# Kernel tuning notes

Hardware: AMD Instinct MI355X
Metric: run time of the kernel (lower is better)

Reference implementation:

```python
import jax, jax.numpy as jnp
import numpy as np

C_NUM, D_NUM = 64, 128
N_NODES = C_NUM * D_NUM + C_NUM + D_NUM  # 8384
HEADS, OUT = 4, 256


def gat_conv(h, src, dst, W, al, ar, b):
    """DGL-style GATConv (eval mode, attn_drop off). h:[N,F], W:[F,H*O], al/ar:[H,O], b:[H*O]."""
    N = h.shape[0]
    H, O = al.shape
    feat = (h @ W).reshape(N, H, O)
    el = jnp.sum(feat * al, axis=-1)                      # [N,H]
    er = jnp.sum(feat * ar, axis=-1)
    e = jax.nn.leaky_relu(el[src] + er[dst], 0.2)         # [E,H]
    m = jax.ops.segment_max(e, dst, num_segments=N)
    m = jnp.where(jnp.isfinite(m), m, 0.0)
    p = jnp.exp(e - m[dst])
    s = jax.ops.segment_sum(p, dst, num_segments=N)
    a = p / jnp.maximum(s[dst], 1e-9)                     # edge softmax per dst, per head
    out = jax.ops.segment_sum(a[:, :, None] * feat[src], dst, num_segments=N)  # [N,H,O]
    return out + b.reshape(1, H, O)


def cagat_layer(edges, dfeat, cvec, gw, al, ar, gb,
                wq_w, wq_b, wk_w, wk_b, wv_w, wv_b, ip_w, ip_b, op_w, op_b):
    ch = cvec.shape[1]
    pad = jnp.repeat(cvec, D_NUM, axis=0)                       # [c*d, ch]
    pad3 = jnp.broadcast_to(cvec.mean(axis=0), (D_NUM, ch))      # [d, ch]
    cfin = jnp.concatenate([pad, cvec, pad3], axis=0)            # [N, ch]
    inf = jnp.concatenate([dfeat, cfin], axis=1)                 # [N, F+ch]
    # 4 relation-specific GATConvs, stacked (HeteroGraphConv aggregate='stack')
    rst = jnp.stack([gat_conv(inf, edges[t, 0], edges[t, 1], gw[t], al[t], ar[t], gb[t])
                     for t in range(4)], axis=1)                 # [N,4,H,O]
    N = inf.shape[0]
    rst = rst.reshape(N, 4 * HEADS, OUT)
    E = OUT
    Q = (cfin @ wq_w + wq_b)[:, None, :]                         # [N,1,E]
    K = rst @ wk_w + wk_b                                        # [N,16,E]
    V = rst @ wv_w + wv_b
    # nn.MultiheadAttention(E, 1): in-proj then single-head SDPA then out-proj
    q = Q @ ip_w[:E].T + ip_b[:E]
    k = K @ ip_w[E:2 * E].T + ip_b[E:2 * E]
    v = V @ ip_w[2 * E:].T + ip_b[2 * E:]
    att = jax.nn.softmax(jnp.einsum('nqe,nke->nqk', q, k) / jnp.sqrt(jnp.float32(E)), axis=-1)
    o = jnp.einsum('nqk,nke->nqe', att, v) @ op_w.T + op_b
    return o.reshape(N, E)


def setup_inputs() -> dict:
    key = jax.random.key(0)
    ks = iter(jax.random.split(key, 64))
    rn = lambda shape: jax.random.normal(next(ks), shape, jnp.float32) * 0.05
    inp = {}
    inp['x'] = rn((D_NUM, 256))
    inp['cf'] = rn((C_NUM, 512))
    inp['cf_net_w'] = rn((512, 128)); inp['cf_net_b'] = rn((128,))
    inp['ht_w'] = rn((512, 256)); inp['ht_b'] = rn((256,))
    for l in ('1', '2'):
        inp['gw' + l] = rn((4, 384, HEADS * OUT))
        inp['al' + l] = rn((4, HEADS, OUT))
        inp['ar' + l] = rn((4, HEADS, OUT))
        inp['gb' + l] = rn((4, HEADS * OUT))
        inp['wq' + l + '_w'] = rn((128, 256)); inp['wq' + l + '_b'] = rn((256,))
        inp['wk' + l + '_w'] = rn((256, 256)); inp['wk' + l + '_b'] = rn((256,))
        inp['wv' + l + '_w'] = rn((256, 256)); inp['wv' + l + '_b'] = rn((256,))
        inp['ip' + l + '_w'] = rn((768, 256)); inp['ip' + l + '_b'] = rn((768,))
        inp['op' + l + '_w'] = rn((256, 256)); inp['op' + l + '_b'] = rn((256,))
    inp['edges'] = jax.random.randint(next(ks), (4, 2, 50000), 0, N_NODES, dtype=jnp.int32)
    return inp


def reference(x, cf, cf_net_w, cf_net_b, ht_w, ht_b,
              gw1, al1, ar1, gb1, wq1_w, wq1_b, wk1_w, wk1_b, wv1_w, wv1_b, ip1_w, ip1_b, op1_w, op1_b,
              gw2, al2, ar2, gb2, wq2_w, wq2_b, wk2_w, wk2_b, wv2_w, wv2_b, ip2_w, ip2_b, op2_w, op2_b,
              edges):
    cf_vec = cf @ cf_net_w + cf_net_b                           # [c, cell_hidden]
    d_pad = jnp.tile(x, (C_NUM, 1))                             # [c*d, in]
    d_uc = cf @ ht_w + ht_b                                     # [c, in]
    d_feat = jnp.concatenate([d_pad, d_uc, x], axis=0)          # [N, in]
    h = cagat_layer(edges, d_feat, cf_vec, gw1, al1, ar1, gb1,
                    wq1_w, wq1_b, wk1_w, wk1_b, wv1_w, wv1_b, ip1_w, ip1_b, op1_w, op1_b)
    h = cagat_layer(edges, h, cf_vec, gw2, al2, ar2, gb2,
                    wq2_w, wq2_b, wk2_w, wk2_b, wv2_w, wv2_b, ip2_w, ip2_b, op2_w, op2_b)
    return h
```

## Files before the change

### kernel.cpp

```cpp
#include <hip/hip_runtime.h>
#include <hip/hip_bf16.h>

typedef __hip_bfloat16 bf16;
typedef __attribute__((ext_vector_type(8))) short short8;
typedef __attribute__((ext_vector_type(4))) short short4v;
typedef __attribute__((ext_vector_type(4))) float f32x4;

#define KN 8384
#define KNPAD 8448
#define KE 50000
#define NBIG 4480

__device__ __forceinline__ float toF(float v){ return v; }
__device__ __forceinline__ float toF(bf16 v){ return __bfloat162float(v); }
__device__ __forceinline__ float b2f(short u){ return __uint_as_float(((unsigned int)(unsigned short)u) << 16); }
__device__ __forceinline__ void stor(float* p, float v){ *p = v; }
__device__ __forceinline__ void stor(bf16* p, float v){ *p = __float2bfloat16(v); }

__device__ __forceinline__ void glds16(const bf16* g, bf16* l){
  __builtin_amdgcn_global_load_lds(
      (const __attribute__((address_space(1))) unsigned int*)(g),
      (__attribute__((address_space(3))) unsigned int*)(l), 16, 0, 0);
}

template<typename TC>
__global__ __launch_bounds__(256)
void gemm_mfma_bt(const bf16* __restrict__ A, const bf16* __restrict__ BT,
                  const float* __restrict__ bias, TC* __restrict__ C,
                  int M, int N, int K, int ldc, int nbx)
{
  __shared__ bf16 As[3][128 * 32];
  __shared__ bf16 Bs[3][128 * 32];
  const int nwg = gridDim.x;
  const int q = nwg >> 3, r = nwg & 7;
  const int xcd = blockIdx.x & 7, idx = blockIdx.x >> 3;
  const int sw = (xcd < r) ? xcd * (q + 1) + idx : r * (q + 1) + (xcd - r) * q + idx;
  const int bn = (sw % nbx) * 128, bm = (sw / nbx) * 128;
  const int tid = threadIdx.x;
  const int w = tid >> 6, l = tid & 63;
  const int wr = (w >> 1) * 64, wc = (w & 1) * 64;
  const int lr = l & 15;
  int rS[2], lqS[2];
  #pragma unroll
  for (int i = 0; i < 2; i++){
    rS[i] = w * 32 + i * 16 + (l >> 2);
    lqS[i] = (l & 3) ^ ((rS[i] >> 1) & 3);
  }
  const bf16* gA0 = A  + (size_t)(bm + rS[0]) * K + lqS[0] * 8;
  const bf16* gA1 = A  + (size_t)(bm + rS[1]) * K + lqS[1] * 8;
  const bf16* gB0 = BT + (size_t)(bn + rS[0]) * K + lqS[0] * 8;
  const bf16* gB1 = BT + (size_t)(bn + rS[1]) * K + lqS[1] * 8;
  const int nt = K >> 5;
  auto issue = [&](int t){
    int b = t - (t / 3) * 3;
    int k0 = t << 5;
    glds16(gA0 + k0, &As[b][w * 1024]);
    glds16(gA1 + k0, &As[b][w * 1024 + 512]);
    glds16(gB0 + k0, &Bs[b][w * 1024]);
    glds16(gB1 + k0, &Bs[b][w * 1024 + 512]);
  };
  f32x4 acc[4][4] = {};
  issue(0);
  issue(1);
  for (int t = 0; t < nt; t++){
    if (t < nt - 1) asm volatile("s_waitcnt vmcnt(4)\ns_barrier" ::: "memory");
    else            asm volatile("s_waitcnt vmcnt(0)\ns_barrier" ::: "memory");
    if (t + 2 < nt) issue(t + 2);
    int b = t - (t / 3) * 3;
    short8 a[4], bb[4];
    #pragma unroll
    for (int i = 0; i < 4; i++){
      int R = wr + i * 16 + lr;
      int pq = (l >> 4) ^ ((R >> 1) & 3);
      a[i] = *(short8*)&As[b][R * 32 + pq * 8];
    }
    #pragma unroll
    for (int j = 0; j < 4; j++){
      int R = wc + j * 16 + lr;
      int pq = (l >> 4) ^ ((R >> 1) & 3);
      bb[j] = *(short8*)&Bs[b][R * 32 + pq * 8];
    }
    #pragma unroll
    for (int i = 0; i < 4; i++)
      #pragma unroll
      for (int j = 0; j < 4; j++)
        acc[i][j] = __builtin_amdgcn_mfma_f32_16x16x32_bf16(a[i], bb[j], acc[i][j], 0, 0, 0);
  }
  const int orow = (l >> 4) * 4, ocol = l & 15;
  #pragma unroll
  for (int i = 0; i < 4; i++){
    #pragma unroll
    for (int j = 0; j < 4; j++){
      int gcol = bn + wc + j * 16 + ocol;
      float bv = bias ? bias[gcol] : 0.f;
      #pragma unroll
      for (int rg = 0; rg < 4; rg++){
        int grow = bm + wr + i * 16 + orow + rg;
        if (grow < M) stor(&C[(size_t)grow * ldc + gcol], acc[i][j][rg] + bv);
      }
    }
  }
}

struct LPtrs {
  const float *gw[2], *al[2], *ar[2];
  const float *wqw[2], *wqb[2], *wkw[2], *wvw[2], *wvb[2];
  const float *ipw[2], *ipb[2], *opw[2], *opb[2];
  bf16* bigBT[2];
  float *ipwQT[2], *wkwT[2], *opwT[2], *wvwT[2];
  float *Wq[2], *B2[2], *M1[2], *bq[2];
  bf16* WvT[2];
  float *bv[2], *biasc[2];
};

#define PT0 1536
#define PT1 4608
#define PT2 4864
#define PT3 5248
#define PT4 5392
__global__ __launch_bounds__(256)
void k_prep_all(LPtrs P){
  const int lay = blockIdx.z;
  const int b = blockIdx.x, tid = threadIdx.x;
  bf16* bigBT = P.bigBT[lay];
  if (b < PT0){
    __shared__ float t[32][33];
    int rel = b / 384, rem = b % 384;
    int n0 = (rem % 32) * 32, k0 = (rem / 32) * 32;
    const float* B = P.gw[lay] + (size_t)rel * 384 * 1024;
    bf16* BT = bigBT + (size_t)rel * 1024 * 384;
    int tx = tid & 31, ty = tid >> 5;
    for (int i = ty; i < 32; i += 8)
      t[i][tx] = B[(size_t)(k0 + i) * 1024 + n0 + tx];
    __syncthreads();
    for (int i = ty; i < 32; i += 8)
      BT[(size_t)(n0 + i) * 384 + k0 + tx] = __float2bfloat16(t[tx][i]);
  } else if (b < PT1){
    int bb = b - PT0;
    int kblk = bb % 96, r = bb / 96;
    int k = kblk * 4 + (tid >> 6), lane = tid & 63;
    int rr = r & 15, t = rr >> 2, h = rr & 3;
    const float* wsrc = ((r < 16) ? P.al[lay] : P.ar[lay]) + t * 1024 + h * 256;
    const float* gp = P.gw[lay] + (size_t)t * 384 * 1024 + (size_t)k * 1024 + h * 256;
    float v = 0.f;
    #pragma unroll
    for (int i = 0; i < 4; i++){
      int o = lane + i * 64;
      v += gp[o] * wsrc[o];
    }
    #pragma unroll
    for (int off = 32; off; off >>= 1) v += __shfl_down(v, off);
    if (lane == 0) bigBT[(size_t)(4352 + r) * 384 + k] = __float2bfloat16(v);
  } else if (b < PT2){
    __shared__ float t[32][33];
    int bb = b - PT1;
    int mat = bb >> 6, rem = bb & 63;
    int c0 = (rem & 7) * 32, r0 = (rem >> 3) * 32;
    const float* S; float* D;
    switch (mat){
      case 0: S = P.ipw[lay]; D = P.ipwQT[lay]; break;
      case 1: S = P.wkw[lay]; D = P.wkwT[lay]; break;
      case 2: S = P.opw[lay]; D = P.opwT[lay]; break;
      default: S = P.wvw[lay]; D = P.wvwT[lay]; break;
    }
    int tx = tid & 31, ty = tid >> 5;
    for (int i = ty; i < 32; i += 8)
      t[i][tx] = S[(size_t)(r0 + i) * 256 + c0 + tx];
    __syncthreads();
    for (int i = ty; i < 32; i += 8)
      D[(size_t)(c0 + i) * 256 + r0 + tx] = t[tx][i];
  } else if (b < PT3){
    int idx = (b - PT2) * 256 + tid;
    bigBT[(size_t)(4096 + idx / 384) * 384 + idx % 384] = __float2bfloat16(0.f);
  } else {
    int idx = (b - PT3) * 256 + tid;
    bigBT[(size_t)(4384 + idx / 384) * 384 + idx % 384] = __float2bfloat16(0.f);
  }
}

__global__ __launch_bounds__(256)
void k_fold1(LPtrs P){
  const int lay = blockIdx.z;
  int b = blockIdx.x, tid = threadIdx.x;
  if (b < 128){
    int c = b; float s = 0.f;
    for (int e = 0; e < 256; e++) s += P.wqw[lay][c * 256 + e] * P.ipwQT[lay][e * 256 + tid];
    P.Wq[lay][c * 256 + tid] = s;
  } else if (b < 384){
    int j = b - 128; float s = 0.f;
    for (int e = 0; e < 256; e++) s += P.wkwT[lay][e * 256 + tid] * P.ipw[lay][(256 + j) * 256 + e];
    P.B2[lay][j * 256 + tid] = s;
  } else if (b < 640){
    int e = b - 384; float s = 0.f;
    for (int f = 0; f < 256; f++) s += P.ipw[lay][(512 + f) * 256 + e] * P.opwT[lay][f * 256 + tid];
    P.M1[lay][e * 256 + tid] = s;
  } else {
    float s = 0.f;
    for (int e = 0; e < 256; e++) s += P.wqb[lay][e] * P.ipwQT[lay][e * 256 + tid];
    P.bq[lay][tid] = s + P.ipb[lay][tid];
  }
}

__global__ __launch_bounds__(256)
void k_fold2(LPtrs P){
  const int lay = blockIdx.z;
  int b = blockIdx.x, tid = threadIdx.x;
  if (b < 256){
    __shared__ float wqr[256];
    wqr[tid] = P.Wq[lay][b * 256 + tid];
    __syncthreads();
    float s = 0.f;
    for (int j = 0; j < 256; j++) s += wqr[j] * P.B2[lay][j * 256 + tid];
    P.bigBT[lay][(size_t)(4096 + tid) * 384 + 256 + b] = __float2bfloat16(s);
  } else if (b < 512){
    int j = b - 256; float s = 0.f;
    for (int e = 0; e < 256; e++) s += P.wvwT[lay][e * 256 + tid] * P.M1[lay][e * 256 + j];
    P.WvT[lay][j * 256 + tid] = __float2bfloat16(s);
  } else {
    float b2 = 0.f;
    for (int j = 0; j < 256; j++) b2 += P.bq[lay][j] * P.B2[lay][j * 256 + tid];
    float s = 0.f;
    for (int e = 0; e < 256; e++) s += P.wvb[lay][e] * P.M1[lay][e * 256 + tid];
    for (int f = 0; f < 256; f++) s += P.ipb[lay][512 + f] * P.opwT[lay][f * 256 + tid];
    P.bv[lay][tid] = s + P.opb[lay][tid];
    for (int i = tid; i < NBIG; i += 256)
      P.biasc[lay][i] = (i - 4096 == tid) ? b2 : 0.f;
  }
}

__global__ __launch_bounds__(384)
void k_pre(const float* __restrict__ cf, const float* __restrict__ cfw, const float* __restrict__ cfb,
           const float* __restrict__ htw, const float* __restrict__ htb,
           float* __restrict__ cfvec, float* __restrict__ duc)
{
  int c = blockIdx.x;
  int col = threadIdx.x;
  __shared__ float row[512];
  for (int i = col; i < 512; i += 384) row[i] = cf[c * 512 + i];
  __syncthreads();
  if (col < 128){
    float acc = cfb[col];
    for (int k = 0; k < 512; k++) acc += row[k] * cfw[k * 128 + col];
    cfvec[c * 128 + col] = acc;
  } else {
    int j = col - 128;
    float acc = htb[j];
    for (int k = 0; k < 512; k++) acc += row[k] * htw[k * 256 + j];
    duc[c * 256 + j] = acc;
  }
}
__global__ void k_mean(const float* cv, float* m){
  int o = threadIdx.x;
  float s = 0.f;
  for (int c = 0; c < 64; c++) s += cv[c * 128 + o];
  m[o] = s * (1.f / 64.f);
}
__global__ __launch_bounds__(384)
void k_infasm(const float* __restrict__ x, const float* __restrict__ duc,
              const float* __restrict__ cv, const float* __restrict__ cm,
              bf16* __restrict__ inf){
  int n = blockIdx.x, o = threadIdx.x;
  float v;
  if (o < 256){
    if (n < 8192)      v = x[(n & 127) * 256 + o];
    else if (n < 8256) v = duc[(n - 8192) * 256 + o];
    else               v = x[(n - 8256) * 256 + o];
  } else {
    int oo = o - 256;
    if (n < 8192)      v = cv[(n >> 7) * 128 + oo];
    else if (n < 8256) v = cv[(n - 8192) * 128 + oo];
    else               v = cm[oo];
  }
  inf[(size_t)n * 384 + o] = __float2bfloat16(v);
}
__global__ void k_zeroi(int* p, int n){
  int i = blockIdx.x * blockDim.x + threadIdx.x; if (i < n) p[i] = 0;
}
__global__ void k_countB(const int* __restrict__ edges, int* __restrict__ cnt){
  int i = blockIdx.x * blockDim.x + threadIdx.x;
  if (i < 4 * KE){
    int t = i / KE, idx = i - t * KE;
    int d = edges[t * 2 * KE + KE + idx];
    atomicAdd(&cnt[t * KN + d], 1);
  }
}
__global__ void k_fillB(const int* __restrict__ edges, int* __restrict__ cur, int* __restrict__ csrc){
  int i = blockIdx.x * blockDim.x + threadIdx.x;
  if (i < 4 * KE){
    int t = i / KE, idx = i - t * KE;
    int s = edges[t * 2 * KE + idx];
    int d = edges[t * 2 * KE + KE + idx];
    int p = atomicAdd(&cur[t * KN + d], 1);
    csrc[p] = s;
  }
}
__global__ void k_scan(const int* __restrict__ cnt, int* __restrict__ ptr,
                       int* __restrict__ cur, int n){
  __shared__ int part[1024];
  int tid = threadIdx.x;
  const int CH = (n + 1023) >> 10;
  int base = tid * CH;
  int s = 0;
  for (int i = 0; i < CH; i++){ int idx = base + i; if (idx < n) s += cnt[idx]; }
  part[tid] = s; __syncthreads();
  for (int off = 1; off < 1024; off <<= 1){
    int v = (tid >= off) ? part[tid - off] : 0;
    __syncthreads();
    part[tid] += v;
    __syncthreads();
  }
  int run = part[tid] - s;
  for (int i = 0; i < CH; i++){
    int idx = base + i;
    if (idx < n){ ptr[idx] = run; cur[idx] = run; run += cnt[idx]; }
  }
  if (tid == 1023) ptr[n] = part[1023];
}

__global__ __launch_bounds__(256)
void k_aggattn(const int* __restrict__ ptr, const int* __restrict__ csrc,
               const bf16* __restrict__ big, const float* __restrict__ gb,
               bf16* __restrict__ rbar)
{
  const int n = blockIdx.x, tid = threadIdx.x;
  const int w = tid >> 6, lane = tid & 63;
  const int t = w;
  const int head = lane >> 4;
  __shared__ float s_rst[16][260];
  __shared__ float s_sc[16];
  __shared__ float sa4[4][64][4];
  __shared__ int ssrcW[4][64];
  const int beg = ptr[t * KN + n], deg = ptr[t * KN + n + 1] - beg;
  short4v e4 = *(const short4v*)&big[(size_t)n * NBIG + 4368 + t * 4];
  float ern[4] = {b2f(e4[0]), b2f(e4[1]), b2f(e4[2]), b2f(e4[3])};
  float sums[4] = {0.f, 0.f, 0.f, 0.f};
  for (int j = lane; j < deg; j += 64){
    int s = csrc[beg + j];
    short4v l4 = *(const short4v*)&big[(size_t)s * NBIG + 4352 + t * 4];
    #pragma unroll
    for (int h = 0; h < 4; h++){
      float e = b2f(l4[h]) + ern[h];
      e = e > 0.f ? e : 0.2f * e;
      sums[h] += __expf(e);
    }
  }
  #pragma unroll
  for (int off = 32; off; off >>= 1){
    #pragma unroll
    for (int h = 0; h < 4; h++) sums[h] += __shfl_xor(sums[h], off);
  }
  float sinv[4];
  #pragma unroll
  for (int h = 0; h < 4; h++) sinv[h] = 1.f / fmaxf(sums[h], 1e-9f);
  float acc[16];
  #pragma unroll
  for (int i = 0; i < 16; i++) acc[i] = 0.f;
  const size_t cbase = (size_t)t * 1024 + lane * 16;
  for (int c0 = 0; c0 < deg; c0 += 64){
    int cn = min(64, deg - c0);
    if (lane < cn){
      int s = csrc[beg + c0 + lane];
      ssrcW[t][lane] = s;
      short4v l4 = *(const short4v*)&big[(size_t)s * NBIG + 4352 + t * 4];
      #pragma unroll
      for (int h = 0; h < 4; h++){
        float e = b2f(l4[h]) + ern[h];
        e = e > 0.f ? e : 0.2f * e;
        sa4[t][lane][h] = __expf(e) * sinv[h];
      }
    }
    int j = 0;
    for (; j + 3 < cn; j += 4){
      int s0 = ssrcW[t][j],     s1 = ssrcW[t][j + 1];
      int s2 = ssrcW[t][j + 2], s3 = ssrcW[t][j + 3];
      float w0 = sa4[t][j][head],     w1 = sa4[t][j + 1][head];
      float w2 = sa4[t][j + 2][head], w3 = sa4[t][j + 3][head];
      const bf16* f0 = &big[(size_t)s0 * NBIG + cbase];
      const bf16* f1 = &big[(size_t)s1 * NBIG + cbase];
      const bf16* f2 = &big[(size_t)s2 * NBIG + cbase];
      const bf16* f3 = &big[(size_t)s3 * NBIG + cbase];
      short8 a0 = *(const short8*)f0, b0 = *(const short8*)(f0 + 8);
      short8 a1 = *(const short8*)f1, b1 = *(const short8*)(f1 + 8);
      short8 a2 = *(const short8*)f2, b2 = *(const short8*)(f2 + 8);
      short8 a3 = *(const short8*)f3, b3 = *(const short8*)(f3 + 8);
      #pragma unroll
      for (int i = 0; i < 8; i++)
        acc[i] += w0 * b2f(a0[i]) + w1 * b2f(a1[i]) + w2 * b2f(a2[i]) + w3 * b2f(a3[i]);
      #pragma unroll
      for (int i = 0; i < 8; i++)
        acc[8 + i] += w0 * b2f(b0[i]) + w1 * b2f(b1[i]) + w2 * b2f(b2[i]) + w3 * b2f(b3[i]);
    }
    for (; j < cn; j++){
      int s = ssrcW[t][j];
      float wj = sa4[t][j][head];
      const bf16* fp = &big[(size_t)s * NBIG + cbase];
      short8 v0 = *(const short8*)fp;
      short8 v1 = *(const short8*)(fp + 8);
      #pragma unroll
      for (int i = 0; i < 8; i++) acc[i] += wj * b2f(v0[i]);
      #pragma unroll
      for (int i = 0; i < 8; i++) acc[8 + i] += wj * b2f(v1[i]);
    }
  }
  {
    const float* gbp = gb + t * 1024 + lane * 16;
    float* rp = &s_rst[t * 4 + head][(lane & 15) * 16];
    #pragma unroll
    for (int i = 0; i < 16; i++) rp[i] = acc[i] + gbp[i];
  }
  __syncthreads();
  const bf16* q = big + (size_t)n * NBIG + 4096;
  #pragma unroll
  for (int si = 0; si < 4; si++){
    int s = w * 4 + si;
    float v = 0.f;
    #pragma unroll
    for (int i = 0; i < 4; i++){
      int o = lane + i * 64;
      v += s_rst[s][o] * toF(q[o]);
    }
    #pragma unroll
    for (int off = 32; off; off >>= 1) v += __shfl_down(v, off);
    if (lane == 0) s_sc[s] = v * 0.0625f;
  }
  __syncthreads();
  float sc[16]; float m = -1e30f;
  #pragma unroll
  for (int s = 0; s < 16; s++){ sc[s] = s_sc[s]; m = fmaxf(m, sc[s]); }
  float sum = 0.f;
  #pragma unroll
  for (int s = 0; s < 16; s++){ sc[s] = __expf(sc[s] - m); sum += sc[s]; }
  float inv = 1.f / sum;
  float r = 0.f;
  #pragma unroll
  for (int s = 0; s < 16; s++) r += sc[s] * s_rst[s][tid];
  rbar[(size_t)n * 256 + tid] = __float2bfloat16(r * inv);
}

extern "C" void kernel_launch(void* const* d_in, const int* in_sizes, int n_in,
                              void* d_out, int out_size, void* d_ws, size_t ws_size,
                              hipStream_t stream)
{
  const float* x   = (const float*)d_in[0];
  const float* cf  = (const float*)d_in[1];
  const float* cfw = (const float*)d_in[2];
  const float* cfb = (const float*)d_in[3];
  const float* htw = (const float*)d_in[4];
  const float* htb = (const float*)d_in[5];
  LPtrs P;
  const float* gbp[2];
  for (int l = 0; l < 2; l++){
    int b = 6 + l * 14;
    P.gw[l]  = (const float*)d_in[b + 0];
    P.al[l]  = (const float*)d_in[b + 1];
    P.ar[l]  = (const float*)d_in[b + 2];
    gbp[l]   = (const float*)d_in[b + 3];
    P.wqw[l] = (const float*)d_in[b + 4];
    P.wqb[l] = (const float*)d_in[b + 5];
    P.wkw[l] = (const float*)d_in[b + 6];
    P.wvw[l] = (const float*)d_in[b + 8];
    P.wvb[l] = (const float*)d_in[b + 9];
    P.ipw[l] = (const float*)d_in[b + 10];
    P.ipb[l] = (const float*)d_in[b + 11];
    P.opw[l] = (const float*)d_in[b + 12];
    P.opb[l] = (const float*)d_in[b + 13];
  }
  const int* edges = (const int*)d_in[34];

  char* w = (char*)d_ws;
  size_t off = 0;
  auto alc = [&](size_t bytes) -> void* {
    off = (off + 255) & ~(size_t)255;
    void* p = w + off; off += bytes; return p;
  };
  float* f_cfvec = (float*)alc(64 * 128 * 4);
  float* f_cfmean= (float*)alc(128 * 4);
  float* f_duc   = (float*)alc(64 * 256 * 4);
  bf16*  b_inf   = (bf16*) alc((size_t)KNPAD * 384 * 2);
  bf16*  b_big   = (bf16*) alc((size_t)KN * NBIG * 2);
  bf16*  b_rbar  = (bf16*) alc((size_t)KNPAD * 256 * 2);
  for (int l = 0; l < 2; l++){
    P.bigBT[l] = (bf16*) alc((size_t)NBIG * 384 * 2);
    P.biasc[l] = (float*)alc((size_t)NBIG * 4);
    P.ipwQT[l] = (float*)alc(256 * 256 * 4);
    P.wkwT[l]  = (float*)alc(256 * 256 * 4);
    P.opwT[l]  = (float*)alc(256 * 256 * 4);
    P.wvwT[l]  = (float*)alc(256 * 256 * 4);
    P.Wq[l]    = (float*)alc(128 * 256 * 4);
    P.B2[l]    = (float*)alc(256 * 256 * 4);
    P.M1[l]    = (float*)alc(256 * 256 * 4);
    P.bq[l]    = (float*)alc(256 * 4);
    P.bv[l]    = (float*)alc(256 * 4);
    P.WvT[l]   = (bf16*) alc(256 * 256 * 2);
  }
  int* i_ptr = (int*)alc((size_t)(4 * KN + 1) * 4);
  int* i_src = (int*)alc((size_t)4 * KE * 4);
  int* i_cnt = (int*)alc((size_t)4 * KN * 4);
  int* i_cur = (int*)alc((size_t)4 * KN * 4);
  if (off > ws_size) return;

  k_pre<<<64, 384, 0, stream>>>(cf, cfw, cfb, htw, htb, f_cfvec, f_duc);
  k_mean<<<1, 128, 0, stream>>>(f_cfvec, f_cfmean);
  k_infasm<<<KN, 384, 0, stream>>>(x, f_duc, f_cfvec, f_cfmean, b_inf);
  k_prep_all<<<dim3(PT4, 1, 2), 256, 0, stream>>>(P);
  k_fold1<<<dim3(641, 1, 2), 256, 0, stream>>>(P);
  k_fold2<<<dim3(513, 1, 2), 256, 0, stream>>>(P);

  k_zeroi<<<(4 * KN + 255) / 256, 256, 0, stream>>>(i_cnt, 4 * KN);
  k_countB<<<(4 * KE + 255) / 256, 256, 0, stream>>>(edges, i_cnt);
  k_scan<<<1, 1024, 0, stream>>>(i_cnt, i_ptr, i_cur, 4 * KN);
  k_fillB<<<(4 * KE + 255) / 256, 256, 0, stream>>>(edges, i_cur, i_src);

  for (int l = 0; l < 2; l++){
    gemm_mfma_bt<bf16><<<(NBIG / 128) * 66, 256, 0, stream>>>(
        b_inf, P.bigBT[l], P.biasc[l], b_big, KN, NBIG, 384, NBIG, NBIG / 128);
    k_aggattn<<<KN, 256, 0, stream>>>(i_ptr, i_src, b_big, gbp[l], b_rbar);
    if (l == 1)
      gemm_mfma_bt<float><<<2 * 66, 256, 0, stream>>>(
          b_rbar, P.WvT[l], P.bv[l], (float*)d_out, KN, 256, 256, 256, 2);
    else
      gemm_mfma_bt<bf16><<<2 * 66, 256, 0, stream>>>(
          b_rbar, P.WvT[l], P.bv[l], b_inf, KN, 256, 256, 384, 2);
  }
}
```

Baseline: 521.0 us.

## Exploit repeated rows of layer-1 input to shrink big GEMM via rank decomposition

Layer-1 input rows for the first 8192 nodes are an x-row concatenated with a cell-vector row, so their projection equals the sum of two small projections. The big layer-1 GEMM over all nodes is replaced by a 192-row GEMM on the distinct x and cell-vector rows plus a 192-row GEMM for the tail nodes, followed by an elementwise expand kernel that adds the pieces and the bias. The count-buffer zeroing is also folded into the prep kernel to drop a launch. This trades GEMM compute for a memory-bound expand pass, and rounding differs slightly because the fp32 partial sums are added before conversion to bf16.

```diff
diff --git a/kernel.cpp b/kernel.cpp
--- a/kernel.cpp
+++ b/kernel.cpp
@@ -111,6 +111,7 @@
   float *Wq[2], *B2[2], *M1[2], *bq[2];
   bf16* WvT[2];
   float *bv[2], *biasc[2];
+  int* cnt;
 };
 
 #define PT0 1536
@@ -118,6 +119,7 @@
 #define PT2 4864
 #define PT3 5248
 #define PT4 5392
+#define PT5 5524
 __global__ __launch_bounds__(256)
 void k_prep_all(LPtrs P){
   const int lay = blockIdx.z;
@@ -172,9 +174,12 @@
   } else if (b < PT3){
     int idx = (b - PT2) * 256 + tid;
     bigBT[(size_t)(4096 + idx / 384) * 384 + idx % 384] = __float2bfloat16(0.f);
-  } else {
+  } else if (b < PT4){
     int idx = (b - PT3) * 256 + tid;
     bigBT[(size_t)(4384 + idx / 384) * 384 + idx % 384] = __float2bfloat16(0.f);
+  } else if (lay == 0){
+    int idx = (b - PT4) * 256 + tid;
+    if (idx < 4 * KN) P.cnt[idx] = 0;
   }
 }
 
@@ -273,8 +278,34 @@
   }
   inf[(size_t)n * 384 + o] = __float2bfloat16(v);
 }
-__global__ void k_zeroi(int* p, int n){
-  int i = blockIdx.x * blockDim.x + threadIdx.x; if (i < n) p[i] = 0;
+__global__ __launch_bounds__(384)
+void k_smallA(const float* __restrict__ x, const float* __restrict__ cv,
+              bf16* __restrict__ A12){
+  int r = blockIdx.x, c = threadIdx.x;
+  float v = 0.f;
+  if (r < 128){
+    if (c < 256) v = x[r * 256 + c];
+  } else if (r < 192){
+    if (c >= 256) v = cv[(r - 128) * 128 + (c - 256)];
+  }
+  A12[(size_t)r * 384 + c] = __float2bfloat16(v);
+}
+__global__ __launch_bounds__(256)
+void k_expand(const float* __restrict__ T12, const float* __restrict__ biasc,
+              bf16* __restrict__ big){
+  int n = blockIdx.x;
+  const float* t1 = T12 + (size_t)(n & 127) * NBIG;
+  const float* t2 = T12 + (size_t)(128 + (n >> 7)) * NBIG;
+  bf16* out = big + (size_t)n * NBIG;
+  for (int c = threadIdx.x * 4; c < NBIG; c += 1024){
+    f32x4 a = *(const f32x4*)&t1[c];
+    f32x4 b = *(const f32x4*)&t2[c];
+    f32x4 bc = *(const f32x4*)&biasc[c];
+    out[c + 0] = __float2bfloat16(a[0] + b[0] + bc[0]);
+    out[c + 1] = __float2bfloat16(a[1] + b[1] + bc[1]);
+    out[c + 2] = __float2bfloat16(a[2] + b[2] + bc[2]);
+    out[c + 3] = __float2bfloat16(a[3] + b[3] + bc[3]);
+  }
 }
 __global__ void k_countB(const int* __restrict__ edges, int* __restrict__ cnt){
   int i = blockIdx.x * blockDim.x + threadIdx.x;
@@ -479,6 +510,8 @@
   bf16*  b_inf   = (bf16*) alc((size_t)KNPAD * 384 * 2);
   bf16*  b_big   = (bf16*) alc((size_t)KN * NBIG * 2);
   bf16*  b_rbar  = (bf16*) alc((size_t)KNPAD * 256 * 2);
+  bf16*  b_A12   = (bf16*) alc((size_t)256 * 384 * 2);
+  float* f_T12   = (float*)alc((size_t)192 * NBIG * 4);
   for (int l = 0; l < 2; l++){
     P.bigBT[l] = (bf16*) alc((size_t)NBIG * 384 * 2);
     P.biasc[l] = (float*)alc((size_t)NBIG * 4);
@@ -497,29 +530,34 @@
   int* i_src = (int*)alc((size_t)4 * KE * 4);
   int* i_cnt = (int*)alc((size_t)4 * KN * 4);
   int* i_cur = (int*)alc((size_t)4 * KN * 4);
+  P.cnt = i_cnt;
   if (off > ws_size) return;
 
   k_pre<<<64, 384, 0, stream>>>(cf, cfw, cfb, htw, htb, f_cfvec, f_duc);
   k_mean<<<1, 128, 0, stream>>>(f_cfvec, f_cfmean);
   k_infasm<<<KN, 384, 0, stream>>>(x, f_duc, f_cfvec, f_cfmean, b_inf);
-  k_prep_all<<<dim3(PT4, 1, 2), 256, 0, stream>>>(P);
+  k_smallA<<<256, 384, 0, stream>>>(x, f_cfvec, b_A12);
+  k_prep_all<<<dim3(PT5, 1, 2), 256, 0, stream>>>(P);
   k_fold1<<<dim3(641, 1, 2), 256, 0, stream>>>(P);
   k_fold2<<<dim3(513, 1, 2), 256, 0, stream>>>(P);
 
-  k_zeroi<<<(4 * KN + 255) / 256, 256, 0, stream>>>(i_cnt, 4 * KN);
   k_countB<<<(4 * KE + 255) / 256, 256, 0, stream>>>(edges, i_cnt);
   k_scan<<<1, 1024, 0, stream>>>(i_cnt, i_ptr, i_cur, 4 * KN);
   k_fillB<<<(4 * KE + 255) / 256, 256, 0, stream>>>(edges, i_cur, i_src);
 
-  for (int l = 0; l < 2; l++){
-    gemm_mfma_bt<bf16><<<(NBIG / 128) * 66, 256, 0, stream>>>(
-        b_inf, P.bigBT[l], P.biasc[l], b_big, KN, NBIG, 384, NBIG, NBIG / 128);
-    k_aggattn<<<KN, 256, 0, stream>>>(i_ptr, i_src, b_big, gbp[l], b_rbar);
-    if (l == 1)
-      gemm_mfma_bt<float><<<2 * 66, 256, 0, stream>>>(
-          b_rbar, P.WvT[l], P.bv[l], (float*)d_out, KN, 256, 256, 256, 2);
-    else
-      gemm_mfma_bt<bf16><<<2 * 66, 256, 0, stream>>>(
-          b_rbar, P.WvT[l], P.bv[l], b_inf, KN, 256, 256, 384, 2);
-  }
-}
+  gemm_mfma_bt<float><<<(NBIG / 128) * 2, 256, 0, stream>>>(
+      b_A12, P.bigBT[0], nullptr, f_T12, 192, NBIG, 384, NBIG, NBIG / 128);
+  gemm_mfma_bt<bf16><<<(NBIG / 128) * 2, 256, 0, stream>>>(
+      b_inf + (size_t)8192 * 384, P.bigBT[0], P.biasc[0],
+      b_big + (size_t)8192 * NBIG, 192, NBIG, 384, NBIG, NBIG / 128);
+  k_expand<<<8192, 256, 0, stream>>>(f_T12, P.biasc[0], b_big);
+  k_aggattn<<<KN, 256, 0, stream>>>(i_ptr, i_src, b_big, gbp[0], b_rbar);
+  gemm_mfma_bt<bf16><<<2 * 66, 256, 0, stream>>>(
+      b_rbar, P.WvT[0], P.bv[0], b_inf, KN, 256, 256, 384, 2);
+
+  gemm_mfma_bt<bf16><<<(NBIG / 128) * 66, 256, 0, stream>>>(
+      b_inf, P.bigBT[1], P.biasc[1], b_big, KN, NBIG, 384, NBIG, NBIG / 128);
+  k_aggattn<<<KN, 256, 0, stream>>>(i_ptr, i_src, b_big, gbp[1], b_rbar);
+  gemm_mfma_bt<float><<<2 * 66, 256, 0, stream>>>(
+      b_rbar, P.WvT[1], P.bv[1], (float*)d_out, KN, 256, 256, 256, 2);
+}
```

After: 503.2 us. 1.04x faster.
